# Optimization experiments

Hardware: AMD Instinct MI355X
Metric: run time of the kernel (lower is better)

The kernel has to match this reference:

```python
import jax, jax.numpy as jnp
import numpy as np
from jax import lax

K = 20  # init kwarg k


def _square_distance(src, dst):
    # src: [B,N,3], dst: [B,M,3] -> [B,N,M] squared euclidean distances
    dist = -2.0 * jnp.einsum('bnd,bmd->bnm', src, dst)
    dist = dist + jnp.sum(src * src, axis=-1)[:, :, None]
    dist = dist + jnp.sum(dst * dst, axis=-1)[:, None, :]
    return dist


def setup_inputs() -> dict:
    key = jax.random.key(0)
    k1, k2 = jax.random.split(key)
    feats = jax.random.normal(k1, (4, 8192, 64), dtype=jnp.float32)
    vertices = jax.random.normal(k2, (4, 8192, 3), dtype=jnp.float32)
    return {"feats": feats, "vertices": vertices}


def reference(feats, vertices):
    # feats is unused in the live forward path of the original module.
    dist = _square_distance(vertices, vertices)          # [B,N,M]
    # torch.topk(dist, k, dim=1, largest=False) -> smallest along N for each query m,
    # then transpose(1,2) -> [B,M,K]. Equivalent: top_k of -dist along last axis of dist^T.
    neg = -jnp.swapaxes(dist, 1, 2)                      # [B,M,N]
    _, idx = lax.top_k(neg, K)                           # [B,M,K] int32 indices into N
    return idx[0]                                        # [M,K] (original selects batch 0)
```

## Files before the change

### kernel.cpp

```cpp
#include <hip/hip_runtime.h>
#include <math.h>

#define KK 20
#define NPTS 8192
#define NQB 8
#define QPL 8
#define NCH 512
#define THREADS 512
#define WIN 2048
#define NWIN 4
#define JPW 4
#define CAP 64
#define MAXC 64
#define MARGIN 4e-3f

__device__ __forceinline__ float norm3(float x, float y, float z) {
    return __fadd_rn(__fadd_rn(__fmul_rn(x, x), __fmul_rn(y, y)), __fmul_rn(z, z));
}

__device__ __forceinline__ float dist_exact(float px, float py, float pz, float pw,
                                            float qx, float qy, float qz, float qn) {
    const float dot = __fadd_rn(
        __fadd_rn(__fmul_rn(pz, qz), __fmul_rn(py, qy)), __fmul_rn(px, qx));
    return __fadd_rn(__fadd_rn(__fmul_rn(dot, -2.0f), pw), qn);
}

__device__ __forceinline__ unsigned omap(float f) {
    const unsigned u = __float_as_uint(f);
    return u ^ (((unsigned)((int)u >> 31)) | 0x80000000u);
}

extern "C" __global__ __launch_bounds__(THREADS, 8)
void knn_kernel(const float* __restrict__ verts, int* __restrict__ out)
{
    __shared__ float vdump[NQB][NCH];
    __shared__ unsigned long long hbk[NQB][CAP];
    __shared__ int cand[NQB][MAXC];

    const int t    = threadIdx.x;
    const int lane = t & 63;
    const int wv   = t >> 6;
    const int c    = t;
    const int qbase = blockIdx.x * NQB;

    float qx2[QPL], qy2[QPL], qz2[QPL];
#pragma unroll
    for (int i = 0; i < QPL; ++i) {
        qx2[i] = -2.0f * verts[(qbase + i) * 3 + 0];
        qy2[i] = -2.0f * verts[(qbase + i) * 3 + 1];
        qz2[i] = -2.0f * verts[(qbase + i) * 3 + 2];
    }

    float mn[QPL];
#pragma unroll
    for (int i = 0; i < QPL; ++i) mn[i] = INFINITY;

    auto pair8 = [&](float px, float py, float pz) {
        const float pw = norm3(px, py, pz);
#pragma unroll
        for (int i = 0; i < QPL; ++i) {
            const float d = __builtin_fmaf(px, qx2[i],
                            __builtin_fmaf(py, qy2[i],
                            __builtin_fmaf(pz, qz2[i], pw)));
            mn[i] = fminf(mn[i], d);
        }
    };

#pragma unroll
    for (int w = 0; w < NWIN; ++w) {
        const float4* vp = (const float4*)(verts + (w * WIN + c * JPW) * 3);
        const float4 A = vp[0], B = vp[1], C = vp[2];
        pair8(A.x, A.y, A.z); pair8(A.w, B.x, B.y);
        pair8(B.z, B.w, C.x); pair8(C.y, C.z, C.w);
    }

#pragma unroll
    for (int i = 0; i < QPL; ++i) vdump[i][c] = mn[i];

    const int qq = wv;
    const int qg2 = qbase + qq;
    const float qxe = verts[qg2 * 3 + 0];
    const float qye = verts[qg2 * 3 + 1];
    const float qze = verts[qg2 * 3 + 2];
    const float qne = norm3(qxe, qye, qze);

    __syncthreads();

    float sv[8];
#pragma unroll
    for (int k = 0; k < 8; ++k) sv[k] = vdump[qq][k * 64 + lane];

    const float m01 = fminf(sv[0], sv[1]), m23 = fminf(sv[2], sv[3]);
    const float m45 = fminf(sv[4], sv[5]), m67 = fminf(sv[6], sv[7]);
    const float lmin = fminf(fminf(m01, m23), fminf(m45, m67));
    const unsigned ul = omap(lmin);
    unsigned A = 0;
#pragma unroll
    for (int b = 31; b >= 10; --b) {
        const unsigned cv = A | (1u << b);
        if (__popcll(__ballot(ul < cv)) <= KK - 1) A = cv;
    }
    A |= 0x3FFu;
    const float Tsh = ((A >> 31) ? __uint_as_float(A ^ 0x80000000u)
                                 : __uint_as_float(~A)) + MARGIN;
    const float T = Tsh + qne;

    int nc = 0;
#pragma unroll
    for (int k = 0; k < 8; ++k) {
        const bool pred = (sv[k] <= Tsh);
        const unsigned long long bal = __ballot(pred);
        const int rank = nc + __popcll(bal & ((1ULL << lane) - 1));
        if (pred && rank < MAXC) cand[qq][rank] = k * 64 + lane;
        nc += __popcll(bal);
    }
    nc = min(nc, MAXC);

    int hc = 0;
    {
        const int sub = lane >> 4;
        const int p = lane & 15;
        const int nfix = (p >> 2) * WIN + (p & 3);
        for (int e0 = 0; e0 < nc; e0 += 16) {
            float PX[4], PY[4], PZ[4]; int NN[4];
#pragma unroll
            for (int u = 0; u < 4; ++u) {
                const int e = e0 + 4 * u + sub;
                const int cc = cand[qq][e < nc ? e : 0];
                const int n = nfix + cc * JPW;
                NN[u] = n;
                PX[u] = verts[n * 3 + 0];
                PY[u] = verts[n * 3 + 1];
                PZ[u] = verts[n * 3 + 2];
            }
#pragma unroll
            for (int u = 0; u < 4; ++u) {
                const float pw = norm3(PX[u], PY[u], PZ[u]);
                const float d = dist_exact(PX[u], PY[u], PZ[u], pw,
                                           qxe, qye, qze, qne);
                const bool pred = ((e0 + 4 * u + sub) < nc) && (d <= T);
                const unsigned long long bal = __ballot(pred);
                const int rank = __popcll(bal & ((1ULL << lane) - 1));
                if (pred) {
                    const int slot = hc + rank;
                    if (slot < CAP)
                        hbk[qq][slot] = ((unsigned long long)omap(d) << 32)
                                      | (unsigned)NN[u];
                }
                hc += __popcll(bal);
            }
        }
    }

    {
        const int kc = min(hc, CAP);
        const unsigned long long mykey = (lane < kc) ? hbk[qq][lane] : ~0ULL;
        int rank = 0;
        for (int e = 0; e < kc; ++e)
            rank += (hbk[qq][e] < mykey) ? 1 : 0;
        if (lane < kc && rank < KK)
            out[(qbase + qq) * KK + rank] =
                (int)(unsigned)(mykey & 0xffffffffULL);
    }
}

extern "C" void kernel_launch(void* const* d_in, const int* in_sizes, int n_in,
                              void* d_out, int out_size, void* d_ws, size_t ws_size,
                              hipStream_t stream) {
    const float* verts = (const float*)d_in[1];
    int* out = (int*)d_out;
    knn_kernel<<<dim3(NPTS / NQB), dim3(THREADS), 0, stream>>>(verts, out);
}
```

Measured before the change: 20.80 us.

## Use contiguous per-thread point chunks and prefetch next candidate batch

Each thread now takes a contiguous chunk of 16 points (12 consecutive float4 loads) instead of 4 points from each of 4 strided windows, and the candidate-to-point mapping changes to match. The rescoring loop also issues the loads for the next batch of 16 candidates before processing the current one, hiding gather latency. The chunk change alters which points share a chunk minimum, which can shift candidate counts, and the prefetch costs extra registers.

Result: slower. 32.93 us (+58.3%).

```diff
diff --git a/kernel.cpp b/kernel.cpp
--- a/kernel.cpp
+++ b/kernel.cpp
@@ -7,9 +7,7 @@
 #define QPL 8
 #define NCH 512
 #define THREADS 512
-#define WIN 2048
-#define NWIN 4
-#define JPW 4
+#define CSZ 16
 #define CAP 64
 #define MAXC 64
 #define MARGIN 4e-3f
@@ -66,12 +64,14 @@
         }
     };
 
+    {
+        const float4* vp = (const float4*)verts + c * 12;
 #pragma unroll
-    for (int w = 0; w < NWIN; ++w) {
-        const float4* vp = (const float4*)(verts + (w * WIN + c * JPW) * 3);
-        const float4 A = vp[0], B = vp[1], C = vp[2];
-        pair8(A.x, A.y, A.z); pair8(A.w, B.x, B.y);
-        pair8(B.z, B.w, C.x); pair8(C.y, C.z, C.w);
+        for (int g = 0; g < 4; ++g) {
+            const float4 A = vp[3 * g + 0], B = vp[3 * g + 1], C = vp[3 * g + 2];
+            pair8(A.x, A.y, A.z); pair8(A.w, B.x, B.y);
+            pair8(B.z, B.w, C.x); pair8(C.y, C.z, C.w);
+        }
     }
 
 #pragma unroll
@@ -120,19 +120,24 @@
     {
         const int sub = lane >> 4;
         const int p = lane & 15;
-        const int nfix = (p >> 2) * WIN + (p & 3);
-        for (int e0 = 0; e0 < nc; e0 += 16) {
-            float PX[4], PY[4], PZ[4]; int NN[4];
+        auto LG = [&](int e0, float* X, float* Y, float* Z, int* N) {
 #pragma unroll
             for (int u = 0; u < 4; ++u) {
                 const int e = e0 + 4 * u + sub;
                 const int cc = cand[qq][e < nc ? e : 0];
-                const int n = nfix + cc * JPW;
-                NN[u] = n;
-                PX[u] = verts[n * 3 + 0];
-                PY[u] = verts[n * 3 + 1];
-                PZ[u] = verts[n * 3 + 2];
+                const int n = cc * CSZ + p;
+                N[u] = n;
+                X[u] = verts[n * 3 + 0];
+                Y[u] = verts[n * 3 + 1];
+                Z[u] = verts[n * 3 + 2];
             }
+        };
+        float PX[4], PY[4], PZ[4]; int PN[4];
+        LG(0, PX, PY, PZ, PN);
+        for (int e0 = 0; e0 < nc; e0 += 16) {
+            float QX[4], QY[4], QZ[4]; int QN[4];
+            const bool more = (e0 + 16) < nc;
+            if (more) LG(e0 + 16, QX, QY, QZ, QN);
 #pragma unroll
             for (int u = 0; u < 4; ++u) {
                 const float pw = norm3(PX[u], PY[u], PZ[u]);
@@ -145,9 +150,15 @@
                     const int slot = hc + rank;
                     if (slot < CAP)
                         hbk[qq][slot] = ((unsigned long long)omap(d) << 32)
-                                      | (unsigned)NN[u];
+                                      | (unsigned)PN[u];
                 }
                 hc += __popcll(bal);
+            }
+            if (more) {
+#pragma unroll
+                for (int u = 0; u < 4; ++u) {
+                    PX[u] = QX[u]; PY[u] = QY[u]; PZ[u] = QZ[u]; PN[u] = QN[u];
+                }
             }
         }
     }
```
